# Kernel optimization log

Measured on AMD Instinct MI355X. Metric: run time of the kernel, lower is better.

The kernel has to match this reference:

```python
import jax, jax.numpy as jnp
import numpy as np

# ---------- filter construction (setup-time, numpy) ----------

def _conv2full(A, B):
    out = np.zeros((A.shape[0] + B.shape[0] - 1, A.shape[1] + B.shape[1] - 1))
    for i in range(B.shape[0]):
        for j in range(B.shape[1]):
            out[i:i + A.shape[0], j:j + A.shape[1]] += B[i, j] * A
    return out

def _mctrans(b, t):
    # McClellan transform of 1-D zero-phase filter b through kernel t
    n = (len(b) - 1) // 2
    c = len(b) // 2
    a = np.concatenate([[b[c]], 2.0 * b[c + 1:]])
    P0 = np.array([[1.0]]); P1 = t
    h = a[1] * t
    h[t.shape[0] // 2, t.shape[1] // 2] += a[0]
    for i in range(2, n + 1):
        P2 = 2.0 * _conv2full(t, P1)
        off = ((P2.shape[0] - P0.shape[0]) // 2, (P2.shape[1] - P0.shape[1]) // 2)
        P2[off[0]:off[0] + P0.shape[0], off[1]:off[1] + P0.shape[1]] -= P0
        hn = a[i] * P2
        o2 = ((P2.shape[0] - h.shape[0]) // 2, (P2.shape[1] - h.shape[1]) // 2)
        hn[o2[0]:o2[0] + h.shape[0], o2[1]:o2[1] + h.shape[1]] += h
        h = hn; P0, P1 = P1, P2
    return h

def _make_filters():
    # pyramidal 'maxflat' 1-D analysis pair (pfilters-style), DC gain sqrt(2)
    k1 = 1.0 - np.sqrt(2.0); k2 = 1.0 / np.sqrt(2.0); k3 = k1; M1 = 1.0 / np.sqrt(2.0)
    hh = np.array([0.25 * k2 * k3, 0.5 * k2, 1.0 + 0.5 * k2 * k3]) * M1
    h = np.concatenate([hh, hh[-2::-1]]) * np.sqrt(2.0)          # 5 taps
    gg = np.array([-0.125 * k1 * k2 * k3, 0.25 * k1 * k2,
                   -0.5 * k1 - 0.5 * k3 - 0.375 * k1 * k2 * k3,
                   1.0 + 0.5 * k1 * k2]) * M1
    g = np.concatenate([gg, gg[-2::-1]]) * np.sqrt(2.0)          # 7 taps
    # diamond maxflat lowpass via McClellan transform of Lagrange halfband
    b = np.array([-1., 0., 9., 16., 9., 0., -1.]) / 32.0
    t = np.array([[0., .25, 0.], [.25, 0., .25], [0., .25, 0.]])
    d0 = _mctrans(b, t)                                           # 7x7 diamond LP
    kh, kw = d0.shape
    mm = (-1.0) ** (np.add.outer(np.arange(kh) - kh // 2, np.arange(kw) - kw // 2))
    d1 = d0 * mm                                                  # complementary diamond
    colmod = (-1.0) ** (np.arange(kw) - kw // 2)                  # diamond -> fan
    f0 = d0 * colmod * np.sqrt(2.0)
    f1 = d1 * colmod * np.sqrt(2.0)
    return h, g, f0, f1

# ---------- jax filtering / resampling primitives ----------

def _sepfilt_per(x, f):
    # separable zero-phase filtering with periodic extension; x [B,C,H,W]
    B, C, H, W = x.shape
    L = f.shape[0]; p = L // 2
    k = f.astype(x.dtype)
    y = jnp.pad(x, ((0, 0), (0, 0), (p, p), (0, 0)), mode='wrap').reshape(B * C, 1, H + 2 * p, W)
    y = jax.lax.conv_general_dilated(y, k.reshape(1, 1, L, 1), (1, 1), 'VALID')
    y = jnp.pad(y, ((0, 0), (0, 0), (0, 0), (p, p)), mode='wrap')
    y = jax.lax.conv_general_dilated(y, k.reshape(1, 1, 1, L), (1, 1), 'VALID')
    return y.reshape(B, C, H, W)

def _filt2_per(x, F):
    B, C, H, W = x.shape
    kh, kw = F.shape; ph, pw = kh // 2, kw // 2
    y = jnp.pad(x, ((0, 0), (0, 0), (ph, ph), (pw, pw)), mode='wrap').reshape(B * C, 1, H + 2 * ph, W + 2 * pw)
    y = jax.lax.conv_general_dilated(y, F.reshape(1, 1, kh, kw).astype(x.dtype), (1, 1), 'VALID')
    return y.reshape(B, C, H, W)

def _qdown_r(x):
    # quincunx downsample: periodic row-shear then keep even rows -> [.., H/2, W]
    H, W = x.shape[-2], x.shape[-1]
    idx = (jnp.arange(W)[None, :] + jnp.arange(H)[:, None]) % W
    z = jnp.take_along_axis(x, jnp.broadcast_to(idx, x.shape), axis=-1)
    return z[..., ::2, :]

def _qdown_c(x):
    # quincunx downsample: periodic column-shear then keep even cols -> [.., H, W/2]
    H, W = x.shape[-2], x.shape[-1]
    idx = (jnp.arange(H)[:, None] + jnp.arange(W)[None, :]) % H
    z = jnp.take_along_axis(x, jnp.broadcast_to(idx, x.shape), axis=-2)
    return z[..., ::2]

# ---------- harness entry points ----------

def setup_inputs() -> dict:
    key = jax.random.key(0)
    x = jax.random.normal(key, (8, 96, 256, 256), dtype=jnp.float32)
    h, g, f0, f1 = _make_filters()
    return {
        'x': x,
        'h': jnp.asarray(h, dtype=jnp.float32),
        'g': jnp.asarray(g, dtype=jnp.float32),
        'f0': jnp.asarray(f0, dtype=jnp.float32),
        'f1': jnp.asarray(f1, dtype=jnp.float32),
    }

def reference(x, h, g, f0, f1):
    # pdfbdec with nlevs=[0,2]: one Laplacian-pyramid level + 2-level DFB on highpass
    xf = _sepfilt_per(x, h)
    xlo = xf[:, :, ::2, ::2]                                  # [B,C,H/2,W/2]
    up = jnp.zeros_like(x).at[:, :, ::2, ::2].set(xlo)
    xhi = x - _sepfilt_per(up, g)                             # LP bandpass [B,C,H,W]
    # DFB level 1: fan filters + quincunx ('1r')
    y0 = _qdown_r(_filt2_per(xhi, f0))                        # [B,C,H/2,W]
    y1 = _qdown_r(_filt2_per(xhi, f1))
    # DFB level 2: transposed fans + quincunx ('2c')
    subs = []
    for y in (y0, y1):
        subs.append(_qdown_c(_filt2_per(y, f0.T)))            # [B,C,H/2,W/2]
        subs.append(_qdown_c(_filt2_per(y, f1.T)))
    xhi_dir = jnp.stack(subs, axis=2)                         # [B,C,4,H/2,W/2]
    return xlo, xhi_dir
```

## Files before the change

### kernel.cpp

```cpp
#include <hip/hip_runtime.h>


#define BC 768

__global__ __launch_bounds__(256) void k1_lowpass(
    const float* __restrict__ x, const float* __restrict__ h,
    float* __restrict__ xlo)
{
    int t = threadIdx.x;
    int tid = blockIdx.x * 256 + t;
    int cb = tid & 63;
    int rb = (tid >> 6) & 63;
    int bc = tid >> 12;
    const float* xb = x + (size_t)bc * 65536;

    int colp[4];
    #pragma unroll
    for (int k = 0; k < 4; ++k) colp[k] = (4 * cb - 2 + 2 * k) & 255;

    float a00 = 0.f, a01 = 0.f, a10 = 0.f, a11 = 0.f;
    #pragma unroll
    for (int pr = 0; pr < 7; ++pr) {
        int row = (4 * rb - 2 + pr) & 255;
        const float* xr = xb + row * 256;
        float X[8];
        #pragma unroll
        for (int k = 0; k < 4; ++k) {
            float2 p = *(const float2*)(xr + colp[k]);
            X[2 * k] = p.x; X[2 * k + 1] = p.y;
        }
        float s0 = h[0]*X[0] + h[1]*X[1] + h[2]*X[2] + h[3]*X[3] + h[4]*X[4];
        float s1 = h[0]*X[2] + h[1]*X[3] + h[2]*X[4] + h[3]*X[5] + h[4]*X[6];
        if (pr <= 4) { a00 += h[pr] * s0;     a01 += h[pr] * s1; }
        if (pr >= 2) { a10 += h[pr - 2] * s0; a11 += h[pr - 2] * s1; }
    }
    size_t ob = (size_t)bc * 16384 + (size_t)(2 * rb) * 128 + 2 * cb;
    *(float2*)(xlo + ob)       = make_float2(a00, a01);
    *(float2*)(xlo + ob + 128) = make_float2(a10, a11);
}

__global__ __launch_bounds__(256) void k2_highpass(
    const float* __restrict__ x, const float* __restrict__ g,
    const float* __restrict__ xlo, float* __restrict__ xs)
{
    int t = threadIdx.x;
    int tid = blockIdx.x * 256 + t;
    int ch = tid & 127;
    int rh = (tid >> 7) & 127;
    int bc = tid >> 14;
    const float* lob = xlo + (size_t)bc * 16384;

    int ri[4] = { (rh - 1) & 127, rh, (rh + 1) & 127, (rh + 2) & 127 };
    int ci[4] = { (ch - 1) & 127, ch, (ch + 1) & 127, (ch + 2) & 127 };

    float ce[4], co[4];
    #pragma unroll
    for (int a = 0; a < 4; ++a) {
        const float* lr = lob + ri[a] * 128;
        float L0 = lr[ci[0]], L1 = lr[ci[1]], L2 = lr[ci[2]], L3 = lr[ci[3]];
        ce[a] = g[1]*L0 + g[3]*L1 + g[5]*L2;
        co[a] = g[0]*L0 + g[2]*L1 + g[4]*L2 + g[6]*L3;
    }
    float aee = g[1]*ce[0] + g[3]*ce[1] + g[5]*ce[2];
    float aeo = g[1]*co[0] + g[3]*co[1] + g[5]*co[2];
    float aoe = g[0]*ce[0] + g[2]*ce[1] + g[4]*ce[2] + g[6]*ce[3];
    float aoo = g[0]*co[0] + g[2]*co[1] + g[4]*co[2] + g[6]*co[3];

    size_t base = (size_t)bc * 65536 + (size_t)(2 * rh) * 256 + 2 * ch;
    float2 xe = *(const float2*)(x + base);
    float2 xo = *(const float2*)(x + base + 256);

    float* xsb = xs + (size_t)bc * 65536;
    int re = 2 * rh, ro = 2 * rh + 1;
    int ce0 = (2 * ch - re + 2) & 255;
    int co0 = (2 * ch - ro + 2) & 255;
    *(float2*)(xsb + re * 256 + ce0) = make_float2(xe.x - aee, xe.y - aeo);
    float* rowo = xsb + ro * 256;
    rowo[co0]             = xo.x - aoe;
    rowo[(co0 + 1) & 255] = xo.y - aoo;
}

__global__ __launch_bounds__(256) void k3_dirfilt(
    const float* __restrict__ xs, const float* __restrict__ f0,
    const float* __restrict__ f1, float* __restrict__ y0,
    float* __restrict__ y1)
{
    int t = threadIdx.x;
    int wb = t & 63;
    int rg = t >> 6;
    int r0 = (blockIdx.x & 15) * 8;
    int bc = blockIdx.x >> 4;
    const float* xsb = xs + (size_t)bc * 65536;

    int base = 2 * r0 + 4 * rg - 3;
    int c0 = (4 * wb - 4) & 255;

    float a0[2][4] = {{0.f,0.f,0.f,0.f},{0.f,0.f,0.f,0.f}};
    float a1[2][4] = {{0.f,0.f,0.f,0.f},{0.f,0.f,0.f,0.f}};

    #pragma unroll
    for (int ro = 0; ro < 9; ++ro) {
        int row = (base + ro) & 255;
        const float* rp = xsb + row * 256;
        float C[16];
        #pragma unroll
        for (int k = 0; k < 4; ++k) {
            float4 v = *(const float4*)(rp + ((c0 + 4 * k) & 255));
            C[4*k] = v.x; C[4*k+1] = v.y; C[4*k+2] = v.z; C[4*k+3] = v.w;
        }
        #pragma unroll
        for (int lr = 0; lr < 2; ++lr) {
            int i = ro - 2 * lr;
            if (i >= 0 && i <= 6) {
                #pragma unroll
                for (int j = 0; j < 7; ++j) {
                    float w0 = f0[i * 7 + j];
                    float w1 = f1[i * 7 + j];
                    int mb = j - ro + 2 * lr + 6;
                    #pragma unroll
                    for (int dw = 0; dw < 4; ++dw) {
                        float v = C[dw + mb];
                        a0[lr][dw] += w0 * v;
                        a1[lr][dw] += w1 * v;
                    }
                }
            }
        }
    }
    #pragma unroll
    for (int lr = 0; lr < 2; ++lr) {
        int r = r0 + 2 * rg + lr;
        size_t o = (size_t)bc * 32768 + (size_t)r * 256 + 4 * wb;
        *(float4*)(y0 + o) = make_float4(a0[lr][0], a0[lr][1], a0[lr][2], a0[lr][3]);
        *(float4*)(y1 + o) = make_float4(a1[lr][0], a1[lr][1], a1[lr][2], a1[lr][3]);
    }
}

#define NCP 80

__global__ __launch_bounds__(256) void k4_qdc(
    const float* __restrict__ ybuf, const float* __restrict__ f0,
    const float* __restrict__ f1, float* __restrict__ out_hi)
{
    __shared__ float tile[128 * NCP];
    int t = threadIdx.x;

    int bx   = blockIdx.x;
    int ccb  = (bx & 3) * 32;
    int yidx = (bx >> 2) & 1;
    int bc   = bx >> 3;
    const float* yb = ybuf + ((size_t)yidx * BC + bc) * 32768;

    int c0 = (2 * ccb - 3 + 256) & 255;

    for (int idx = t; idx < 128 * 70; idx += 256) {
        int rr = idx / 70;
        int cc = idx - rr * 70;
        tile[rr * NCP + cc] = yb[rr * 256 + ((c0 + cc) & 255)];
    }
    __syncthreads();

    int lc = t & 31;
    int lh = t >> 5;
    int cc = ccb + lc;
    int cbase = 2 * lc;
    int rbase = (16 * lh + 2 * cc - 3 + 128) & 127;

    float s0[16], s1[16];
    #pragma unroll
    for (int m = 0; m < 16; ++m) { s0[m] = 0.f; s1[m] = 0.f; }

    #pragma unroll
    for (int RR = 0; RR < 22; ++RR) {
        const float* tr = &tile[((rbase + RR) & 127) * NCP + cbase];
        float T[8];
        #pragma unroll
        for (int k = 0; k < 4; ++k) {
            float2 u = *(const float2*)(tr + 2 * k);
            T[2*k] = u.x; T[2*k+1] = u.y;
        }
        #pragma unroll
        for (int m = 0; m < 16; ++m) {
            int i = RR - m;
            if (i >= 0 && i <= 6) {
                #pragma unroll
                for (int j = 0; j < 7; ++j) {
                    s0[m] += f0[j * 7 + i] * T[j];
                    s1[m] += f1[j * 7 + i] * T[j];
                }
            }
        }
    }
    #pragma unroll
    for (int m = 0; m < 16; ++m) {
        int hh = 16 * lh + m;
        size_t o = (size_t)bc * 65536 + (size_t)(2 * yidx) * 16384
                 + (size_t)hh * 128 + cc;
        out_hi[o]         = s0[m];
        out_hi[o + 16384] = s1[m];
    }
}

extern "C" void kernel_launch(void* const* d_in, const int* in_sizes, int n_in,
                              void* d_out, int out_size, void* d_ws, size_t ws_size,
                              hipStream_t stream)
{
    const float* x  = (const float*)d_in[0];
    const float* h  = (const float*)d_in[1];
    const float* g  = (const float*)d_in[2];
    const float* f0 = (const float*)d_in[3];
    const float* f1 = (const float*)d_in[4];

    float* out   = (float*)d_out;
    float* xlo   = out;
    float* hireg = out + 12582912;
    float* ybuf  = (float*)d_ws;

    k1_lowpass<<<12288, 256, 0, stream>>>(x, h, xlo);
    k2_highpass<<<49152, 256, 0, stream>>>(x, g, xlo, hireg);
    k3_dirfilt<<<12288, 256, 0, stream>>>(hireg, f0, f1, ybuf, ybuf + 25165824);
    k4_qdc<<<6144, 256, 0, stream>>>(ybuf, f0, f1, hireg);
}
```

Measured before the change: 716.2 us.

## Fuse DFB level-1 and level-2 filtering into one kernel via LDS-resident intermediate

Merges the first directional filtering stage and the second transposed-fan stage into a single kernel. Each 1024-thread block computes one half-image of y0 or y1 for one channel into 128 KB of shared memory and then runs the level-2 filters directly from LDS. This removes the global-memory round trip for the y buffers and one launch. In exchange there is one block per CU with heavy LDS use, which lowers occupancy and latency hiding. The sheared intermediate now goes to workspace instead of the output region.

```diff
diff --git a/kernel.cpp b/kernel.cpp
--- a/kernel.cpp
+++ b/kernel.cpp
@@ -80,124 +80,102 @@
     rowo[(co0 + 1) & 255] = xo.y - aoo;
 }
 
-__global__ __launch_bounds__(256) void k3_dirfilt(
+__global__ __launch_bounds__(1024) void k34_fused(
     const float* __restrict__ xs, const float* __restrict__ f0,
-    const float* __restrict__ f1, float* __restrict__ y0,
-    float* __restrict__ y1)
-{
+    const float* __restrict__ f1, float* __restrict__ out_hi)
+{
+    __shared__ float ylds[128 * 256];
     int t = threadIdx.x;
-    int wb = t & 63;
-    int rg = t >> 6;
-    int r0 = (blockIdx.x & 15) * 8;
-    int bc = blockIdx.x >> 4;
+    int yidx = blockIdx.x & 1;
+    int bc   = blockIdx.x >> 1;
     const float* xsb = xs + (size_t)bc * 65536;
-
-    int base = 2 * r0 + 4 * rg - 3;
-    int c0 = (4 * wb - 4) & 255;
-
-    float a0[2][4] = {{0.f,0.f,0.f,0.f},{0.f,0.f,0.f,0.f}};
-    float a1[2][4] = {{0.f,0.f,0.f,0.f},{0.f,0.f,0.f,0.f}};
-
-    #pragma unroll
-    for (int ro = 0; ro < 9; ++ro) {
-        int row = (base + ro) & 255;
-        const float* rp = xsb + row * 256;
-        float C[16];
-        #pragma unroll
-        for (int k = 0; k < 4; ++k) {
-            float4 v = *(const float4*)(rp + ((c0 + 4 * k) & 255));
-            C[4*k] = v.x; C[4*k+1] = v.y; C[4*k+2] = v.z; C[4*k+3] = v.w;
-        }
-        #pragma unroll
-        for (int lr = 0; lr < 2; ++lr) {
-            int i = ro - 2 * lr;
-            if (i >= 0 && i <= 6) {
-                #pragma unroll
-                for (int j = 0; j < 7; ++j) {
-                    float w0 = f0[i * 7 + j];
-                    float w1 = f1[i * 7 + j];
-                    int mb = j - ro + 2 * lr + 6;
+    const float* fy = yidx ? f1 : f0;
+
+    {
+        int wb = t & 63;
+        int rg = t >> 6;
+        int r0 = rg * 8;
+        int c0 = (4 * wb - 4) & 255;
+
+        float acc[8][4];
+        #pragma unroll
+        for (int lr = 0; lr < 8; ++lr)
+            #pragma unroll
+            for (int d = 0; d < 4; ++d) acc[lr][d] = 0.f;
+
+        int base = 2 * r0 - 3;
+        #pragma unroll
+        for (int ro = 0; ro < 21; ++ro) {
+            int row = (base + ro + 256) & 255;
+            const float* rp = xsb + row * 256;
+            float C[16];
+            #pragma unroll
+            for (int k = 0; k < 4; ++k) {
+                float4 v = *(const float4*)(rp + ((c0 + 4 * k) & 255));
+                C[4*k] = v.x; C[4*k+1] = v.y; C[4*k+2] = v.z; C[4*k+3] = v.w;
+            }
+            #pragma unroll
+            for (int lr = 0; lr < 8; ++lr) {
+                int i = ro - 2 * lr;
+                if (i >= 0 && i <= 6) {
                     #pragma unroll
-                    for (int dw = 0; dw < 4; ++dw) {
-                        float v = C[dw + mb];
-                        a0[lr][dw] += w0 * v;
-                        a1[lr][dw] += w1 * v;
+                    for (int j = 0; j < 7; ++j) {
+                        float w0 = fy[i * 7 + j];
+                        int mb = j - i + 6;
+                        #pragma unroll
+                        for (int d = 0; d < 4; ++d)
+                            acc[lr][d] += w0 * C[d + mb];
                     }
                 }
             }
         }
-    }
-    #pragma unroll
-    for (int lr = 0; lr < 2; ++lr) {
-        int r = r0 + 2 * rg + lr;
-        size_t o = (size_t)bc * 32768 + (size_t)r * 256 + 4 * wb;
-        *(float4*)(y0 + o) = make_float4(a0[lr][0], a0[lr][1], a0[lr][2], a0[lr][3]);
-        *(float4*)(y1 + o) = make_float4(a1[lr][0], a1[lr][1], a1[lr][2], a1[lr][3]);
-    }
-}
-
-#define NCP 80
-
-__global__ __launch_bounds__(256) void k4_qdc(
-    const float* __restrict__ ybuf, const float* __restrict__ f0,
-    const float* __restrict__ f1, float* __restrict__ out_hi)
-{
-    __shared__ float tile[128 * NCP];
-    int t = threadIdx.x;
-
-    int bx   = blockIdx.x;
-    int ccb  = (bx & 3) * 32;
-    int yidx = (bx >> 2) & 1;
-    int bc   = bx >> 3;
-    const float* yb = ybuf + ((size_t)yidx * BC + bc) * 32768;
-
-    int c0 = (2 * ccb - 3 + 256) & 255;
-
-    for (int idx = t; idx < 128 * 70; idx += 256) {
-        int rr = idx / 70;
-        int cc = idx - rr * 70;
-        tile[rr * NCP + cc] = yb[rr * 256 + ((c0 + cc) & 255)];
+        #pragma unroll
+        for (int lr = 0; lr < 8; ++lr) {
+            *(float4*)(&ylds[(r0 + lr) * 256 + 4 * wb]) =
+                make_float4(acc[lr][0], acc[lr][1], acc[lr][2], acc[lr][3]);
+        }
     }
     __syncthreads();
 
-    int lc = t & 31;
-    int lh = t >> 5;
-    int cc = ccb + lc;
-    int cbase = 2 * lc;
-    int rbase = (16 * lh + 2 * cc - 3 + 128) & 127;
-
-    float s0[16], s1[16];
-    #pragma unroll
-    for (int m = 0; m < 16; ++m) { s0[m] = 0.f; s1[m] = 0.f; }
-
-    #pragma unroll
-    for (int RR = 0; RR < 22; ++RR) {
-        const float* tr = &tile[((rbase + RR) & 127) * NCP + cbase];
-        float T[8];
-        #pragma unroll
-        for (int k = 0; k < 4; ++k) {
-            float2 u = *(const float2*)(tr + 2 * k);
-            T[2*k] = u.x; T[2*k+1] = u.y;
+    {
+        int cc = t & 127;
+        int lh = t >> 7;
+        int rbase = (16 * lh + 2 * cc - 3 + 128) & 127;
+        int cb64 = (2 * cc - 4) & 255;
+
+        float s0[16], s1[16];
+        #pragma unroll
+        for (int m = 0; m < 16; ++m) { s0[m] = 0.f; s1[m] = 0.f; }
+
+        #pragma unroll
+        for (int RR = 0; RR < 22; ++RR) {
+            const float* tr = &ylds[((rbase + RR) & 127) * 256];
+            float T[8];
+            #pragma unroll
+            for (int k = 0; k < 4; ++k) {
+                float2 u = *(const float2*)(tr + ((cb64 + 2 * k) & 255));
+                T[2*k] = u.x; T[2*k+1] = u.y;
+            }
+            #pragma unroll
+            for (int m = 0; m < 16; ++m) {
+                int i = RR - m;
+                if (i >= 0 && i <= 6) {
+                    #pragma unroll
+                    for (int j = 0; j < 7; ++j) {
+                        s0[m] += f0[j * 7 + i] * T[j + 1];
+                        s1[m] += f1[j * 7 + i] * T[j + 1];
+                    }
+                }
+            }
         }
         #pragma unroll
         for (int m = 0; m < 16; ++m) {
-            int i = RR - m;
-            if (i >= 0 && i <= 6) {
-                #pragma unroll
-                for (int j = 0; j < 7; ++j) {
-                    s0[m] += f0[j * 7 + i] * T[j];
-                    s1[m] += f1[j * 7 + i] * T[j];
-                }
-            }
-        }
-    }
-    #pragma unroll
-    for (int m = 0; m < 16; ++m) {
-        int hh = 16 * lh + m;
-        size_t o = (size_t)bc * 65536 + (size_t)(2 * yidx) * 16384
-                 + (size_t)hh * 128 + cc;
-        out_hi[o]         = s0[m];
-        out_hi[o + 16384] = s1[m];
+            int hh = 16 * lh + m;
+            size_t o = (size_t)bc * 65536 + (size_t)(2 * yidx) * 16384
+                     + (size_t)hh * 128 + cc;
+            out_hi[o]         = s0[m];
+            out_hi[o + 16384] = s1[m];
+        }
     }
 }
 
@@ -214,10 +192,9 @@
     float* out   = (float*)d_out;
     float* xlo   = out;
     float* hireg = out + 12582912;
-    float* ybuf  = (float*)d_ws;
+    float* xsbuf = (float*)d_ws;
 
     k1_lowpass<<<12288, 256, 0, stream>>>(x, h, xlo);
-    k2_highpass<<<49152, 256, 0, stream>>>(x, g, xlo, hireg);
-    k3_dirfilt<<<12288, 256, 0, stream>>>(hireg, f0, f1, ybuf, ybuf + 25165824);
-    k4_qdc<<<6144, 256, 0, stream>>>(ybuf, f0, f1, hireg);
-}
+    k2_highpass<<<49152, 256, 0, stream>>>(x, g, xlo, xsbuf);
+    k34_fused<<<1536, 1024, 0, stream>>>(xsbuf, f0, f1, hireg);
+}
```

Measured after the change: 670.4 us. 1.07x faster.
